# Kernel optimization log

Hardware: AMD Instinct MI355X
Metric: run time of the kernel (lower is better)

Reference implementation:

```python
import jax, jax.numpy as jnp
import numpy as np

S, N, H, O = 128, 2048, 128, 128  # seq_len(=input_size), num_samples, hidden_size, output_size


def setup_inputs() -> dict:
    key = jax.random.key(0)
    ks = jax.random.split(key, 7)
    scale = 1.0 / np.sqrt(H)
    u = lambda k, shp: jax.random.uniform(k, shp, jnp.float32, -scale, scale)
    return {
        "x": jax.random.normal(ks[0], (S, N, H), jnp.float32),
        "W_ih": u(ks[1], (4 * H, H)),   # PyTorch gate order: i, f, g, o
        "W_hh": u(ks[2], (4 * H, H)),
        "b_ih": u(ks[3], (4 * H,)),
        "b_hh": u(ks[4], (4 * H,)),
        "W_out": u(ks[5], (O, H)),
        "b_out": u(ks[6], (O,)),
    }


def _lstm_forward(x, W_ih, W_hh, b_ih, b_hh, W_out, b_out):
    n, h = x.shape[1], W_hh.shape[1]
    # Precompute input contribution to gates for all timesteps: [S, N, 4H]
    xg = jnp.einsum("snh,gh->sng", x, W_ih) + (b_ih + b_hh)

    def step(carry, xt):
        h_t, c_t = carry
        gates = xt + h_t @ W_hh.T  # [N, 4H]
        i, f, g, o = jnp.split(gates, 4, axis=-1)
        i = jax.nn.sigmoid(i)
        f = jax.nn.sigmoid(f)
        g = jnp.tanh(g)
        o = jax.nn.sigmoid(o)
        c_t = f * c_t + i * g
        h_t = o * jnp.tanh(c_t)
        return (h_t, c_t), h_t

    h0 = jnp.zeros((n, h), x.dtype)  # init_hidden(): zeros
    c0 = jnp.zeros((n, h), x.dtype)
    _, out = jax.lax.scan(step, (h0, c0), xg)  # out: [S, N, H]
    # Linear projection fused over all timesteps
    pred = jnp.einsum("snh,oh->sno", out, W_out) + b_out  # [S, N, O]
    return pred


def reference(x, W_ih, W_hh, b_ih, b_hh, W_out, b_out):
    return _lstm_forward(x, W_ih, W_hh, b_ih, b_hh, W_out, b_out)
```

## Files before the change

kernel.cpp:

```cpp
#include <hip/hip_runtime.h>
#include <hip/hip_bf16.h>


#define S_LEN   128
#define N_BATCH 2048
#define H_DIM   128
#define O_DIM   128

using short8  = __attribute__((ext_vector_type(8))) short;
using short4v = __attribute__((ext_vector_type(4))) short;
using floatx4 = __attribute__((ext_vector_type(4))) float;
typedef unsigned short u16;

#define ROWP     264
#define BUFELEMS (16 * ROWP)

__device__ __forceinline__ u16 f2b(float f) {
    unsigned int u = __float_as_uint(f);
    return (u16)((u + 0x7FFF + ((u >> 16) & 1)) >> 16);
}
__device__ __forceinline__ short8 pack8(const float* p) {
    short8 r;
#pragma unroll
    for (int i = 0; i < 8; ++i) r[i] = (short)f2b(p[i]);
    return r;
}
__device__ __forceinline__ short4v pack4(float4 f) {
    short4v r;
    r[0] = (short)f2b(f.x); r[1] = (short)f2b(f.y);
    r[2] = (short)f2b(f.z); r[3] = (short)f2b(f.w);
    return r;
}
__device__ __forceinline__ float sigmoidf_fast(float v) {
    return __builtin_amdgcn_rcpf(1.0f + __builtin_amdgcn_exp2f(-1.4426950408889634f * v));
}
__device__ __forceinline__ float tanhf_fast(float v) {
    return 1.0f - 2.0f * __builtin_amdgcn_rcpf(1.0f + __builtin_amdgcn_exp2f(2.8853900817779268f * v));
}

__device__ __forceinline__ void lds_barrier() {
    asm volatile("s_waitcnt lgkmcnt(0)" ::: "memory");
    __builtin_amdgcn_s_barrier();
}

__global__ __launch_bounds__(512, 2)
void lstm_persist(const float* __restrict__ x,
                  const float* __restrict__ W_ih,
                  const float* __restrict__ W_hh,
                  const float* __restrict__ b_ih,
                  const float* __restrict__ b_hh,
                  const float* __restrict__ W_out,
                  const float* __restrict__ b_out,
                  float* __restrict__ pred) {
    __shared__ short sh[2 * BUFELEMS];

    const int tid  = (int)threadIdx.x;
    const int wave = tid >> 6;
    const int lane = tid & 63;
    const int quad = lane >> 4;
    const int l15  = lane & 15;
    const int n0   = (int)blockIdx.x * 16;

    short8 wx[4][4], wh[4][4], wo[4];
    float  biasv[4];
#pragma unroll
    for (int t = 0; t < 4; ++t) {
        const int g = t * 128 + wave * 16 + l15;
#pragma unroll
        for (int kk = 0; kk < 4; ++kk) {
            wx[t][kk] = pack8(W_ih + g * H_DIM + kk * 32 + quad * 8);
            wh[t][kk] = pack8(W_hh + g * H_DIM + kk * 32 + quad * 8);
        }
        biasv[t] = b_ih[g] + b_hh[g];
    }
    const int ocol = wave * 16 + l15;
#pragma unroll
    for (int kk = 0; kk < 4; ++kk)
        wo[kk] = pack8(W_out + ocol * H_DIM + kk * 32 + quad * 8);
    const float bo = b_out[ocol];

    const int xm = tid >> 5;
    const int xq = (tid & 31) * 4;

    for (int i = tid; i < 16 * 128; i += 512)
        sh[(i >> 7) * ROWP + 128 + (i & 127)] = 0;
    {
        float4 f0 = *reinterpret_cast<const float4*>(x + ((size_t)(n0 + xm)) * H_DIM + xq);
        float4 f1 = *reinterpret_cast<const float4*>(x + ((size_t)N_BATCH + n0 + xm) * H_DIM + xq);
        *reinterpret_cast<short4v*>(&sh[BUFELEMS + xm * ROWP + xq]) = pack4(f0);
        *reinterpret_cast<short4v*>(&sh[xm * ROWP + xq]) = pack4(f1);
    }
    float4 xcur = *reinterpret_cast<const float4*>(x + ((size_t)2 * N_BATCH + n0 + xm) * H_DIM + xq);
    float4 xnext = *reinterpret_cast<const float4*>(x + ((size_t)3 * N_BATCH + n0 + xm) * H_DIM + xq);
    __syncthreads();

    const int arow = l15 * ROWP + quad * 8;
    const int hcol = 128 + wave * 16 + l15;

    floatx4 xg0 = {biasv[0], biasv[0], biasv[0], biasv[0]};
    floatx4 xg1 = {biasv[1], biasv[1], biasv[1], biasv[1]};
    floatx4 xg2 = {biasv[2], biasv[2], biasv[2], biasv[2]};
    floatx4 xg3 = {biasv[3], biasv[3], biasv[3], biasv[3]};
#pragma unroll
    for (int kk = 0; kk < 4; ++kk) {
        short8 a = *reinterpret_cast<const short8*>(&sh[BUFELEMS + arow + kk * 32]);
        xg0 = __builtin_amdgcn_mfma_f32_16x16x32_bf16(a, wx[0][kk], xg0, 0, 0, 0);
        xg1 = __builtin_amdgcn_mfma_f32_16x16x32_bf16(a, wx[1][kk], xg1, 0, 0, 0);
        xg2 = __builtin_amdgcn_mfma_f32_16x16x32_bf16(a, wx[2][kk], xg2, 0, 0, 0);
        xg3 = __builtin_amdgcn_mfma_f32_16x16x32_bf16(a, wx[3][kk], xg3, 0, 0, 0);
    }
    __syncthreads();

    float cc[4] = {0.f, 0.f, 0.f, 0.f};

    for (int s = 0; s < S_LEN; ++s) {
        short* shb = sh + (s & 1) * BUFELEMS;
        short* shn = sh + ((s & 1) ^ 1) * BUFELEMS;

        floatx4 g0 = xg0, g1 = xg1, g2 = xg2, g3 = xg3;
        floatx4 ao = {bo, bo, bo, bo};

#pragma unroll
        for (int kk = 0; kk < 4; ++kk) {
            short8 ah = *reinterpret_cast<const short8*>(&shb[arow + 128 + kk * 32]);
            g0 = __builtin_amdgcn_mfma_f32_16x16x32_bf16(ah, wh[0][kk], g0, 0, 0, 0);
            g1 = __builtin_amdgcn_mfma_f32_16x16x32_bf16(ah, wh[1][kk], g1, 0, 0, 0);
            g2 = __builtin_amdgcn_mfma_f32_16x16x32_bf16(ah, wh[2][kk], g2, 0, 0, 0);
            g3 = __builtin_amdgcn_mfma_f32_16x16x32_bf16(ah, wh[3][kk], g3, 0, 0, 0);
            ao = __builtin_amdgcn_mfma_f32_16x16x32_bf16(ah, wo[kk], ao, 0, 0, 0);
        }

        if (s > 0) {
            size_t base = ((size_t)(s - 1) * N_BATCH + n0 + quad * 4) * O_DIM + wave * 16 + l15;
#pragma unroll
            for (int r = 0; r < 4; ++r)
                pred[base + (size_t)r * O_DIM] = ao[r];
        }

        xg0 = floatx4{biasv[0], biasv[0], biasv[0], biasv[0]};
        xg1 = floatx4{biasv[1], biasv[1], biasv[1], biasv[1]};
        xg2 = floatx4{biasv[2], biasv[2], biasv[2], biasv[2]};
        xg3 = floatx4{biasv[3], biasv[3], biasv[3], biasv[3]};
#pragma unroll
        for (int kk = 0; kk < 4; ++kk) {
            short8 axv = *reinterpret_cast<const short8*>(&shb[arow + kk * 32]);
            xg0 = __builtin_amdgcn_mfma_f32_16x16x32_bf16(axv, wx[0][kk], xg0, 0, 0, 0);
            xg1 = __builtin_amdgcn_mfma_f32_16x16x32_bf16(axv, wx[1][kk], xg1, 0, 0, 0);
            xg2 = __builtin_amdgcn_mfma_f32_16x16x32_bf16(axv, wx[2][kk], xg2, 0, 0, 0);
            xg3 = __builtin_amdgcn_mfma_f32_16x16x32_bf16(axv, wx[3][kk], xg3, 0, 0, 0);
        }

        if (s <= 125)
            *reinterpret_cast<short4v*>(&shn[xm * ROWP + xq]) = pack4(xcur);
        if (s <= 124)
            xnext = *reinterpret_cast<const float4*>(
                x + ((size_t)(s + 3) * N_BATCH + n0 + xm) * H_DIM + xq);

        float hv[4];
#pragma unroll
        for (int r = 0; r < 4; ++r) {
            float iv = sigmoidf_fast(g0[r]);
            float fv = sigmoidf_fast(g1[r]);
            float gv = tanhf_fast(g2[r]);
            float ov = sigmoidf_fast(g3[r]);
            cc[r] = fv * cc[r] + iv * gv;
            hv[r] = ov * tanhf_fast(cc[r]);
        }
#pragma unroll
        for (int r = 0; r < 4; ++r)
            shn[(quad * 4 + r) * ROWP + hcol] = (short)f2b(hv[r]);

        xcur = xnext;
        lds_barrier();
    }

    floatx4 ao = {bo, bo, bo, bo};
#pragma unroll
    for (int kk = 0; kk < 4; ++kk) {
        short8 ah = *reinterpret_cast<const short8*>(&sh[arow + 128 + kk * 32]);
        ao = __builtin_amdgcn_mfma_f32_16x16x32_bf16(ah, wo[kk], ao, 0, 0, 0);
    }
    size_t base = ((size_t)(S_LEN - 1) * N_BATCH + n0 + quad * 4) * O_DIM + wave * 16 + l15;
#pragma unroll
    for (int r = 0; r < 4; ++r)
        pred[base + (size_t)r * O_DIM] = ao[r];
}

extern "C" void kernel_launch(void* const* d_in, const int* in_sizes, int n_in,
                              void* d_out, int out_size, void* d_ws, size_t ws_size,
                              hipStream_t stream) {
    const float* x    = (const float*)d_in[0];
    const float* Wih  = (const float*)d_in[1];
    const float* Whh  = (const float*)d_in[2];
    const float* bih  = (const float*)d_in[3];
    const float* bhh  = (const float*)d_in[4];
    const float* Wout = (const float*)d_in[5];
    const float* bout = (const float*)d_in[6];
    float* pred = (float*)d_out;

    lstm_persist<<<dim3(N_BATCH / 16), dim3(512), 0, stream>>>(
        x, Wih, Whh, bih, bhh, Wout, bout, pred);
}
```

Measured before the change: 358.8 us.

## Load x fragments directly from global into MFMA registers, drop LDS staging

Removes the LDS staging of x. Each lane now loads its own MFMA A-fragment of x for the next timestep straight from global memory, issuing the loads early in the step and converting to bf16 just before the input-projection MFMAs. The LDS buffer shrinks to hold only h, with padded rows. This saves LDS stores and reads and the two-step register prefetch chain, but each wave now fetches all of x redundantly (8 waves per block) and global latency sits within a single step instead of being hidden two steps ahead.

```diff
diff --git a/kernel.cpp b/kernel.cpp
--- a/kernel.cpp
+++ b/kernel.cpp
@@ -8,12 +8,11 @@
 #define O_DIM   128
 
 using short8  = __attribute__((ext_vector_type(8))) short;
-using short4v = __attribute__((ext_vector_type(4))) short;
 using floatx4 = __attribute__((ext_vector_type(4))) float;
 typedef unsigned short u16;
 
-#define ROWP     264
-#define BUFELEMS (16 * ROWP)
+#define HP   136
+#define HBUF (16 * HP)
 
 __device__ __forceinline__ u16 f2b(float f) {
     unsigned int u = __float_as_uint(f);
@@ -25,10 +24,12 @@
     for (int i = 0; i < 8; ++i) r[i] = (short)f2b(p[i]);
     return r;
 }
-__device__ __forceinline__ short4v pack4(float4 f) {
-    short4v r;
-    r[0] = (short)f2b(f.x); r[1] = (short)f2b(f.y);
-    r[2] = (short)f2b(f.z); r[3] = (short)f2b(f.w);
+__device__ __forceinline__ short8 cvt8(float4 a, float4 b) {
+    short8 r;
+    r[0] = (short)f2b(a.x); r[1] = (short)f2b(a.y);
+    r[2] = (short)f2b(a.z); r[3] = (short)f2b(a.w);
+    r[4] = (short)f2b(b.x); r[5] = (short)f2b(b.y);
+    r[6] = (short)f2b(b.z); r[7] = (short)f2b(b.w);
     return r;
 }
 __device__ __forceinline__ float sigmoidf_fast(float v) {
@@ -52,7 +53,7 @@
                   const float* __restrict__ W_out,
                   const float* __restrict__ b_out,
                   float* __restrict__ pred) {
-    __shared__ short sh[2 * BUFELEMS];
+    __shared__ short sh[2 * HBUF];
 
     const int tid  = (int)threadIdx.x;
     const int wave = tid >> 6;
@@ -79,23 +80,11 @@
         wo[kk] = pack8(W_out + ocol * H_DIM + kk * 32 + quad * 8);
     const float bo = b_out[ocol];
 
-    const int xm = tid >> 5;
-    const int xq = (tid & 31) * 4;
+    const float*  xb    = x + (size_t)(n0 + l15) * H_DIM + quad * 8;
+    const size_t  xstep = (size_t)N_BATCH * H_DIM;
 
     for (int i = tid; i < 16 * 128; i += 512)
-        sh[(i >> 7) * ROWP + 128 + (i & 127)] = 0;
-    {
-        float4 f0 = *reinterpret_cast<const float4*>(x + ((size_t)(n0 + xm)) * H_DIM + xq);
-        float4 f1 = *reinterpret_cast<const float4*>(x + ((size_t)N_BATCH + n0 + xm) * H_DIM + xq);
-        *reinterpret_cast<short4v*>(&sh[BUFELEMS + xm * ROWP + xq]) = pack4(f0);
-        *reinterpret_cast<short4v*>(&sh[xm * ROWP + xq]) = pack4(f1);
-    }
-    float4 xcur = *reinterpret_cast<const float4*>(x + ((size_t)2 * N_BATCH + n0 + xm) * H_DIM + xq);
-    float4 xnext = *reinterpret_cast<const float4*>(x + ((size_t)3 * N_BATCH + n0 + xm) * H_DIM + xq);
-    __syncthreads();
-
-    const int arow = l15 * ROWP + quad * 8;
-    const int hcol = 128 + wave * 16 + l15;
+        sh[(i >> 7) * HP + (i & 127)] = 0;
 
     floatx4 xg0 = {biasv[0], biasv[0], biasv[0], biasv[0]};
     floatx4 xg1 = {biasv[1], biasv[1], biasv[1], biasv[1]};
@@ -103,26 +92,44 @@
     floatx4 xg3 = {biasv[3], biasv[3], biasv[3], biasv[3]};
 #pragma unroll
     for (int kk = 0; kk < 4; ++kk) {
-        short8 a = *reinterpret_cast<const short8*>(&sh[BUFELEMS + arow + kk * 32]);
-        xg0 = __builtin_amdgcn_mfma_f32_16x16x32_bf16(a, wx[0][kk], xg0, 0, 0, 0);
-        xg1 = __builtin_amdgcn_mfma_f32_16x16x32_bf16(a, wx[1][kk], xg1, 0, 0, 0);
-        xg2 = __builtin_amdgcn_mfma_f32_16x16x32_bf16(a, wx[2][kk], xg2, 0, 0, 0);
-        xg3 = __builtin_amdgcn_mfma_f32_16x16x32_bf16(a, wx[3][kk], xg3, 0, 0, 0);
+        float4 a = *reinterpret_cast<const float4*>(xb + kk * 32);
+        float4 b = *reinterpret_cast<const float4*>(xb + kk * 32 + 4);
+        short8 xf = cvt8(a, b);
+        xg0 = __builtin_amdgcn_mfma_f32_16x16x32_bf16(xf, wx[0][kk], xg0, 0, 0, 0);
+        xg1 = __builtin_amdgcn_mfma_f32_16x16x32_bf16(xf, wx[1][kk], xg1, 0, 0, 0);
+        xg2 = __builtin_amdgcn_mfma_f32_16x16x32_bf16(xf, wx[2][kk], xg2, 0, 0, 0);
+        xg3 = __builtin_amdgcn_mfma_f32_16x16x32_bf16(xf, wx[3][kk], xg3, 0, 0, 0);
     }
     __syncthreads();
 
     float cc[4] = {0.f, 0.f, 0.f, 0.f};
+    const int arow = l15 * HP + quad * 8;
+    const int hcol = wave * 16 + l15;
 
     for (int s = 0; s < S_LEN; ++s) {
-        short* shb = sh + (s & 1) * BUFELEMS;
-        short* shn = sh + ((s & 1) ^ 1) * BUFELEMS;
+        short* shb = sh + (s & 1) * HBUF;
+        short* shn = sh + ((s & 1) ^ 1) * HBUF;
+        const bool   ldx = (s < S_LEN - 1);
+        const float* xs1 = xb + (size_t)(s + 1) * xstep;
 
         floatx4 g0 = xg0, g1 = xg1, g2 = xg2, g3 = xg3;
         floatx4 ao = {bo, bo, bo, bo};
 
+        float4 xr0, xr1, xr2, xr3, xr4, xr5, xr6, xr7;
+        if (ldx) {
+            xr0 = *reinterpret_cast<const float4*>(xs1 + 0);
+            xr1 = *reinterpret_cast<const float4*>(xs1 + 4);
+            xr2 = *reinterpret_cast<const float4*>(xs1 + 32);
+            xr3 = *reinterpret_cast<const float4*>(xs1 + 36);
+            xr4 = *reinterpret_cast<const float4*>(xs1 + 64);
+            xr5 = *reinterpret_cast<const float4*>(xs1 + 68);
+            xr6 = *reinterpret_cast<const float4*>(xs1 + 96);
+            xr7 = *reinterpret_cast<const float4*>(xs1 + 100);
+        }
+
 #pragma unroll
         for (int kk = 0; kk < 4; ++kk) {
-            short8 ah = *reinterpret_cast<const short8*>(&shb[arow + 128 + kk * 32]);
+            short8 ah = *reinterpret_cast<const short8*>(&shb[arow + kk * 32]);
             g0 = __builtin_amdgcn_mfma_f32_16x16x32_bf16(ah, wh[0][kk], g0, 0, 0, 0);
             g1 = __builtin_amdgcn_mfma_f32_16x16x32_bf16(ah, wh[1][kk], g1, 0, 0, 0);
             g2 = __builtin_amdgcn_mfma_f32_16x16x32_bf16(ah, wh[2][kk], g2, 0, 0, 0);
@@ -137,24 +144,32 @@
                 pred[base + (size_t)r * O_DIM] = ao[r];
         }
 
-        xg0 = floatx4{biasv[0], biasv[0], biasv[0], biasv[0]};
-        xg1 = floatx4{biasv[1], biasv[1], biasv[1], biasv[1]};
-        xg2 = floatx4{biasv[2], biasv[2], biasv[2], biasv[2]};
-        xg3 = floatx4{biasv[3], biasv[3], biasv[3], biasv[3]};
-#pragma unroll
-        for (int kk = 0; kk < 4; ++kk) {
-            short8 axv = *reinterpret_cast<const short8*>(&shb[arow + kk * 32]);
-            xg0 = __builtin_amdgcn_mfma_f32_16x16x32_bf16(axv, wx[0][kk], xg0, 0, 0, 0);
-            xg1 = __builtin_amdgcn_mfma_f32_16x16x32_bf16(axv, wx[1][kk], xg1, 0, 0, 0);
-            xg2 = __builtin_amdgcn_mfma_f32_16x16x32_bf16(axv, wx[2][kk], xg2, 0, 0, 0);
-            xg3 = __builtin_amdgcn_mfma_f32_16x16x32_bf16(axv, wx[3][kk], xg3, 0, 0, 0);
-        }
-
-        if (s <= 125)
-            *reinterpret_cast<short4v*>(&shn[xm * ROWP + xq]) = pack4(xcur);
-        if (s <= 124)
-            xnext = *reinterpret_cast<const float4*>(
-                x + ((size_t)(s + 3) * N_BATCH + n0 + xm) * H_DIM + xq);
+        if (ldx) {
+            short8 xf0 = cvt8(xr0, xr1);
+            short8 xf1 = cvt8(xr2, xr3);
+            short8 xf2 = cvt8(xr4, xr5);
+            short8 xf3 = cvt8(xr6, xr7);
+            xg0 = floatx4{biasv[0], biasv[0], biasv[0], biasv[0]};
+            xg1 = floatx4{biasv[1], biasv[1], biasv[1], biasv[1]};
+            xg2 = floatx4{biasv[2], biasv[2], biasv[2], biasv[2]};
+            xg3 = floatx4{biasv[3], biasv[3], biasv[3], biasv[3]};
+            xg0 = __builtin_amdgcn_mfma_f32_16x16x32_bf16(xf0, wx[0][0], xg0, 0, 0, 0);
+            xg1 = __builtin_amdgcn_mfma_f32_16x16x32_bf16(xf0, wx[1][0], xg1, 0, 0, 0);
+            xg2 = __builtin_amdgcn_mfma_f32_16x16x32_bf16(xf0, wx[2][0], xg2, 0, 0, 0);
+            xg3 = __builtin_amdgcn_mfma_f32_16x16x32_bf16(xf0, wx[3][0], xg3, 0, 0, 0);
+            xg0 = __builtin_amdgcn_mfma_f32_16x16x32_bf16(xf1, wx[0][1], xg0, 0, 0, 0);
+            xg1 = __builtin_amdgcn_mfma_f32_16x16x32_bf16(xf1, wx[1][1], xg1, 0, 0, 0);
+            xg2 = __builtin_amdgcn_mfma_f32_16x16x32_bf16(xf1, wx[2][1], xg2, 0, 0, 0);
+            xg3 = __builtin_amdgcn_mfma_f32_16x16x32_bf16(xf1, wx[3][1], xg3, 0, 0, 0);
+            xg0 = __builtin_amdgcn_mfma_f32_16x16x32_bf16(xf2, wx[0][2], xg0, 0, 0, 0);
+            xg1 = __builtin_amdgcn_mfma_f32_16x16x32_bf16(xf2, wx[1][2], xg1, 0, 0, 0);
+            xg2 = __builtin_amdgcn_mfma_f32_16x16x32_bf16(xf2, wx[2][2], xg2, 0, 0, 0);
+            xg3 = __builtin_amdgcn_mfma_f32_16x16x32_bf16(xf2, wx[3][2], xg3, 0, 0, 0);
+            xg0 = __builtin_amdgcn_mfma_f32_16x16x32_bf16(xf3, wx[0][3], xg0, 0, 0, 0);
+            xg1 = __builtin_amdgcn_mfma_f32_16x16x32_bf16(xf3, wx[1][3], xg1, 0, 0, 0);
+            xg2 = __builtin_amdgcn_mfma_f32_16x16x32_bf16(xf3, wx[2][3], xg2, 0, 0, 0);
+            xg3 = __builtin_amdgcn_mfma_f32_16x16x32_bf16(xf3, wx[3][3], xg3, 0, 0, 0);
+        }
 
         float hv[4];
 #pragma unroll
@@ -168,16 +183,15 @@
         }
 #pragma unroll
         for (int r = 0; r < 4; ++r)
-            shn[(quad * 4 + r) * ROWP + hcol] = (short)f2b(hv[r]);
-
-        xcur = xnext;
+            shn[(quad * 4 + r) * HP + hcol] = (short)f2b(hv[r]);
+
         lds_barrier();
     }
 
     floatx4 ao = {bo, bo, bo, bo};
 #pragma unroll
     for (int kk = 0; kk < 4; ++kk) {
-        short8 ah = *reinterpret_cast<const short8*>(&sh[arow + 128 + kk * 32]);
+        short8 ah = *reinterpret_cast<const short8*>(&sh[arow + kk * 32]);
         ao = __builtin_amdgcn_mfma_f32_16x16x32_bf16(ah, wo[kk], ao, 0, 0, 0);
     }
     size_t base = ((size_t)(S_LEN - 1) * N_BATCH + n0 + quad * 4) * O_DIM + wave * 16 + l15;
```

After: 559.9 us. 1.56x slower.
